# Performance work log

Hardware: AMD Instinct MI355X
Metric: run time of the kernel (lower is better)

## Reference

```python
import jax, jax.numpy as jnp
import numpy as np

WIN = 8          # current_window
PRETRAIN = 8     # pretrain_window
HEADS = 8
SHIFT = WIN // 2 # shift_size, shift_dir = [1, 1] (shift_mode=1)
L = WIN * WIN
LOG100 = float(np.log(100.0))


def _shift_mask(H, W):
    # bands (shift_dir=[1,1], no padding). Pairs from different regions get -100.
    hr = np.repeat(np.arange(3), [H - WIN, WIN - SHIFT, SHIFT])
    wr = np.repeat(np.arange(3), [W - WIN, WIN - SHIFT, SHIFT])
    region = hr[:, None] * 3 + wr[None, :]                      # [H, W]
    reg = region.reshape(H // WIN, WIN, W // WIN, WIN)
    reg = reg.transpose(0, 2, 1, 3).reshape(-1, L)              # [nw, L]
    m = np.where(reg[:, :, None] != reg[:, None, :], -100.0, 0.0)
    return jnp.asarray(m, dtype=jnp.float32)[None, :, None]     # [1, nw, 1, L, L]


def _rel_bias(cpb_w1, cpb_b1, cpb_w2):
    # Swin-v2 continuous relative position bias (log-spaced coords + MLP).
    pos = np.stack(np.meshgrid(np.arange(WIN), np.arange(WIN), indexing='ij'), -1).reshape(L, 2)
    rc = (pos[:, None, :] - pos[None, :, :]).astype(np.float32)  # [L, L, 2]
    rc = rc / (PRETRAIN - 1) * 8.0
    rc = np.sign(rc) * np.log2(np.abs(rc) + 1.0) / np.log2(8.0)
    rc = jnp.asarray(rc)
    bias = jax.nn.relu(rc @ cpb_w1 + cpb_b1) @ cpb_w2            # [L, L, heads]
    bias = 16.0 * jax.nn.sigmoid(bias)
    return bias.transpose(2, 0, 1)                               # [heads, L, L]


def _l2n(a):
    # tf.math.l2_normalize with epsilon=1.55e-5
    return a * jax.lax.rsqrt(jnp.maximum(jnp.sum(a * a, -1, keepdims=True), 1.55e-5))


def setup_inputs() -> dict:
    key = jax.random.key(0)
    ks = jax.random.split(key, 6)
    B, H, W, C = 16, 128, 128, 256
    cpb = 512
    return {
        'x': jax.random.normal(ks[0], (B, H, W, C), jnp.float32),
        'qkv_w': jax.random.normal(ks[1], (C, 3 * C), jnp.float32) * 0.02,
        'q_bias': jnp.zeros((C,), jnp.float32),
        'v_bias': jnp.zeros((C,), jnp.float32),
        'scale': jnp.full((HEADS, 1, 1), np.log(10.0), jnp.float32),
        'cpb_w1': jax.random.normal(ks[2], (2, cpb), jnp.float32) * 0.02,
        'cpb_b1': jnp.zeros((cpb,), jnp.float32),
        'cpb_w2': jax.random.normal(ks[3], (cpb, HEADS), jnp.float32) * 0.02,
        'proj_w': jax.random.normal(ks[4], (C, C), jnp.float32) * 0.02,
        'proj_b': jnp.zeros((C,), jnp.float32),
    }


def reference(x, qkv_w, q_bias, v_bias, scale, cpb_w1, cpb_b1, cpb_w2, proj_w, proj_b):
    B, H, W, C = x.shape
    units = C // HEADS
    # qkv 1x1 conv + (q, 0, v) bias
    bias = jnp.concatenate([q_bias, jnp.zeros_like(q_bias), v_bias])
    qkv = jnp.einsum('bhwc,cd->bhwd', x, qkv_w) + bias
    # cyclic shift (H, W > window so shift is applied; no padding needed)
    qkv = jnp.roll(qkv, (-SHIFT, -SHIFT), axis=(1, 2))
    # fused window partition -> [B, nw, heads, L, 3*units]
    nh, nw = H // WIN, W // WIN
    t = qkv.reshape(B, nh, WIN, nw, WIN, HEADS, 3 * units)
    t = t.transpose(0, 1, 3, 5, 2, 4, 6).reshape(B, nh * nw, HEADS, L, 3 * units)
    q, k, v = jnp.split(t, 3, axis=-1)
    # cosine attention with clamped learned logit scale
    logit_scale = jnp.exp(jnp.minimum(scale, LOG100))            # [heads, 1, 1]
    attn = jnp.einsum('bnhld,bnhmd->bnhlm', _l2n(q) * logit_scale, _l2n(k))
    attn = attn + _rel_bias(cpb_w1, cpb_b1, cpb_w2)[None, None] + _shift_mask(H, W)
    attn = jax.nn.softmax(attn, axis=-1)
    out = jnp.einsum('bnhlm,bnhmd->bnhld', attn, v)
    # reverse partition, reverse shift, output projection
    out = out.reshape(B, nh, nw, HEADS, WIN, WIN, units)
    out = out.transpose(0, 1, 4, 2, 5, 3, 6).reshape(B, H, W, C)
    out = jnp.roll(out, (SHIFT, SHIFT), axis=(1, 2))
    return jnp.einsum('bhwc,cd->bhwd', out, proj_w) + proj_b
```

## Files before the change

kernel.cpp:

```cpp
#include <hip/hip_runtime.h>

typedef __attribute__((ext_vector_type(4))) float  f32x4;
typedef __attribute__((ext_vector_type(8))) __bf16 bf16x8;
typedef __attribute__((ext_vector_type(4))) __bf16 bf16x4;

__global__ __launch_bounds__(256) void wprep_kernel(const float* __restrict__ qw,
                                                    const float* __restrict__ pw,
                                                    const float* __restrict__ qb,
                                                    const float* __restrict__ vb,
                                                    __bf16* __restrict__ W2,
                                                    __bf16* __restrict__ Wp,
                                                    float* __restrict__ bcat) {
  int i = blockIdx.x * 256 + threadIdx.x;
  if (i < 24576) {
    int h = i / 3072, rem = i - h * 3072;
    int ft = rem >> 9, rem2 = rem & 511;
    int ks = rem2 >> 6, l = rem2 & 63;
    int g = l >> 4, c = l & 15;
    int col = h * 96 + ft * 16 + c;
    bf16x8 v;
    #pragma unroll
    for (int j = 0; j < 8; ++j)
      v[j] = (__bf16)qw[(ks * 32 + g * 8 + j) * 768 + col];
    *(bf16x8*)(W2 + (size_t)i * 8) = v;
  } else if (i < 24576 + 8192) {
    int j = i - 24576;
    int wv = j >> 10, rem = j & 1023;
    int ft = rem >> 9, rem2 = rem & 511;
    int ks = rem2 >> 6, l = rem2 & 63;
    int g = l >> 4, c = l & 15;
    int col = wv * 32 + ft * 16 + c;
    bf16x8 v;
    #pragma unroll
    for (int j8 = 0; j8 < 8; ++j8)
      v[j8] = (__bf16)pw[(ks * 32 + g * 8 + j8) * 256 + col];
    *(bf16x8*)(Wp + (size_t)j * 8) = v;
  } else if (i < 24576 + 8192 + 768) {
    int cdx = i - 24576 - 8192;
    bcat[cdx] = (cdx < 256) ? qb[cdx] : ((cdx < 512) ? 0.0f : vb[cdx - 512]);
  }
}

__global__ __launch_bounds__(256) void cpb_kernel(const float* __restrict__ w1,
                                                  const float* __restrict__ b1,
                                                  const float* __restrict__ w2,
                                                  float* __restrict__ bias) {
  int pair = blockIdx.x * 256 + threadIdx.x;
  int lq = pair >> 6, mk = pair & 63;
  float d0 = (float)((lq >> 3) - (mk >> 3));
  float d1 = (float)((lq & 7) - (mk & 7));
  float v0 = d0 * (8.0f / 7.0f);
  float v1 = d1 * (8.0f / 7.0f);
  float s0 = (v0 > 0.f) ? 1.f : ((v0 < 0.f) ? -1.f : 0.f);
  float s1 = (v1 > 0.f) ? 1.f : ((v1 < 0.f) ? -1.f : 0.f);
  float r0 = s0 * log2f(fabsf(v0) + 1.0f) * (1.0f / 3.0f);
  float r1 = s1 * log2f(fabsf(v1) + 1.0f) * (1.0f / 3.0f);
  float acc[8] = {0.f, 0.f, 0.f, 0.f, 0.f, 0.f, 0.f, 0.f};
  #pragma unroll 4
  for (int j = 0; j < 512; ++j) {
    float h = fmaxf(r0 * w1[j] + r1 * w1[512 + j] + b1[j], 0.0f);
    #pragma unroll
    for (int q = 0; q < 8; ++q) acc[q] += h * w2[j * 8 + q];
  }
  #pragma unroll
  for (int q = 0; q < 8; ++q) {
    float s = 16.0f / (1.0f + __expf(-acc[q]));
    bias[(q * 64 + lq) * 64 + mk] = s;
  }
}

__device__ __forceinline__ int win_region(int tok, int wi, int wj) {
  int r = tok >> 3, cc = tok & 7;
  int rh = (wi == 15) ? ((r < 4) ? 1 : 2) : 0;
  int rw = (wj == 15) ? ((cc < 4) ? 1 : 2) : 0;
  return rh * 3 + rw;
}

__global__ __launch_bounds__(512, 2) void fused_kernel(
    const float* __restrict__ x, const __bf16* __restrict__ W2,
    const __bf16* __restrict__ Wp, const float* __restrict__ bcat,
    const float* __restrict__ scale, const float* __restrict__ cpb,
    const float* __restrict__ pb, float* __restrict__ outf)
{
  __shared__ __align__(16) __bf16 xs[64 * 256];
  __shared__ __align__(16) __bf16 vst[8][64 * 36];
  const f32x4 zz = {0.f, 0.f, 0.f, 0.f};

  int t = threadIdx.x;
  int h = t >> 6, l = t & 63, g = l >> 4, c = l & 15;
  int win = blockIdx.x, b = blockIdx.y;
  int wi = win >> 4, wj = win & 15;
  bool edge = (wi == 15) || (wj == 15);

  {
    int r = t >> 3;
    int q8 = t & 7;
    int ht = (wi * 8 + (r >> 3) + 4) & 127;
    int wt = (wj * 8 + (r & 7) + 4) & 127;
    const float* src = x + (size_t)((b * 128 + ht) * 128 + wt) * 256 + q8 * 32;
    #pragma unroll
    for (int q = 0; q < 4; ++q) {
      f32x4 a0 = *(const f32x4*)(src + q * 8);
      f32x4 a1 = *(const f32x4*)(src + q * 8 + 4);
      bf16x8 v;
      #pragma unroll
      for (int j = 0; j < 4; ++j) { v[j] = (__bf16)a0[j]; v[4 + j] = (__bf16)a1[j]; }
      int phys = (q8 * 4 + q) ^ (r & 7);
      *(bf16x8*)&xs[r * 256 + phys * 8] = v;
    }
  }
  __syncthreads();

  int toko[4];
  #pragma unroll
  for (int i = 0; i < 4; ++i) {
    int tok = 16 * i + c;
    int ht = (wi * 8 + (tok >> 3) + 4) & 127;
    int wt = (wj * 8 + (tok & 7) + 4) & 127;
    toko[i] = ((b * 128 + ht) * 128 + wt) * 256;
  }

  const __bf16* Wh = W2 + (size_t)h * 24576;
  float ls = __expf(fminf(scale[h], 4.6051701859880914f));

  bf16x8 kA[4], qB[4];
  {
    f32x4 aqk[4][4];
    #pragma unroll
    for (int ft = 0; ft < 4; ++ft)
      #pragma unroll
      for (int tt = 0; tt < 4; ++tt) aqk[ft][tt] = zz;

    #pragma unroll
    for (int ks = 0; ks < 8; ++ks) {
      bf16x8 wf[4], xf[4];
      #pragma unroll
      for (int ft = 0; ft < 4; ++ft)
        wf[ft] = *(const bf16x8*)(Wh + (size_t)((ft * 8 + ks) * 64 + l) * 8);
      #pragma unroll
      for (int tt = 0; tt < 4; ++tt) {
        int phys = (ks * 4 + g) ^ (c & 7);
        xf[tt] = *(const bf16x8*)&xs[(tt * 16 + c) * 256 + phys * 8];
      }
      #pragma unroll
      for (int ft = 0; ft < 4; ++ft)
        #pragma unroll
        for (int tt = 0; tt < 4; ++tt)
          aqk[ft][tt] = __builtin_amdgcn_mfma_f32_16x16x32_bf16(wf[ft], xf[tt], aqk[ft][tt], 0, 0, 0);
    }

    #pragma unroll
    for (int ft = 0; ft < 4; ++ft) {
      f32x4 bb = *(const f32x4*)&bcat[h * 96 + ft * 16 + 4 * g];
      #pragma unroll
      for (int tt = 0; tt < 4; ++tt) aqk[ft][tt] += bb;
    }

    #pragma unroll
    for (int tt = 0; tt < 4; ++tt) {
      float sq = 0.f, sk = 0.f;
      #pragma unroll
      for (int i = 0; i < 4; ++i) {
        sq += aqk[0][tt][i] * aqk[0][tt][i] + aqk[1][tt][i] * aqk[1][tt][i];
        sk += aqk[2][tt][i] * aqk[2][tt][i] + aqk[3][tt][i] * aqk[3][tt][i];
      }
      sq += __shfl_xor(sq, 16); sq += __shfl_xor(sq, 32);
      sk += __shfl_xor(sk, 16); sk += __shfl_xor(sk, 32);
      float rq = rsqrtf(fmaxf(sq, 1.55e-5f)) * ls;
      float rk = rsqrtf(fmaxf(sk, 1.55e-5f));
      #pragma unroll
      for (int i = 0; i < 4; ++i) {
        qB[tt][i]     = (__bf16)(aqk[0][tt][i] * rq);
        qB[tt][4 + i] = (__bf16)(aqk[1][tt][i] * rq);
        kA[tt][i]     = (__bf16)(aqk[2][tt][i] * rk);
        kA[tt][4 + i] = (__bf16)(aqk[3][tt][i] * rk);
      }
    }
  }

  {
    f32x4 av[2][4];
    #pragma unroll
    for (int ft = 0; ft < 2; ++ft)
      #pragma unroll
      for (int tt = 0; tt < 4; ++tt) av[ft][tt] = zz;

    #pragma unroll
    for (int ks = 0; ks < 8; ++ks) {
      bf16x8 wf[2], xf[4];
      #pragma unroll
      for (int ft = 0; ft < 2; ++ft)
        wf[ft] = *(const bf16x8*)(Wh + (size_t)(((4 + ft) * 8 + ks) * 64 + l) * 8);
      #pragma unroll
      for (int tt = 0; tt < 4; ++tt) {
        int phys = (ks * 4 + g) ^ (c & 7);
        xf[tt] = *(const bf16x8*)&xs[(tt * 16 + c) * 256 + phys * 8];
      }
      #pragma unroll
      for (int ft = 0; ft < 2; ++ft)
        #pragma unroll
        for (int tt = 0; tt < 4; ++tt)
          av[ft][tt] = __builtin_amdgcn_mfma_f32_16x16x32_bf16(wf[ft], xf[tt], av[ft][tt], 0, 0, 0);
    }
    __syncthreads();

    f32x4 bb4 = *(const f32x4*)&bcat[h * 96 + 64 + 4 * g];
    f32x4 bb5 = *(const f32x4*)&bcat[h * 96 + 80 + 4 * g];
    #pragma unroll
    for (int tt = 0; tt < 4; ++tt) {
      bf16x4 v0, v1;
      #pragma unroll
      for (int i = 0; i < 4; ++i) {
        v0[i] = (__bf16)(av[0][tt][i] + bb4[i]);
        v1[i] = (__bf16)(av[1][tt][i] + bb5[i]);
      }
      __bf16* vrow = &vst[h][(tt * 16 + c) * 36];
      *(bf16x4*)&vrow[4 * g]      = v0;
      *(bf16x4*)&vrow[16 + 4 * g] = v1;
    }
  }

  bf16x8 va[2][2];
  #pragma unroll
  for (int mh = 0; mh < 2; ++mh)
    #pragma unroll
    for (int kp = 0; kp < 2; ++kp)
      #pragma unroll
      for (int j = 0; j < 8; ++j)
        va[mh][kp][j] =
            vst[h][(32 * kp + 16 * (j >> 2) + 4 * g + (j & 3)) * 36 + 16 * mh + c];

  #pragma unroll
  for (int nt = 0; nt < 4; ++nt) {
    f32x4 tt4[4];
    #pragma unroll
    for (int mt = 0; mt < 4; ++mt)
      tt4[mt] = __builtin_amdgcn_mfma_f32_16x16x32_bf16(kA[mt], qB[nt], zz, 0, 0, 0);
    int q = nt * 16 + c;
    float p[16];
    #pragma unroll
    for (int mt = 0; mt < 4; ++mt) {
      f32x4 bb = *(const f32x4*)&cpb[(h * 64 + q) * 64 + mt * 16 + 4 * g];
      #pragma unroll
      for (int i = 0; i < 4; ++i) p[mt * 4 + i] = tt4[mt][i] + bb[i];
    }
    if (edge) {
      int regq = win_region(q, wi, wj);
      #pragma unroll
      for (int mt = 0; mt < 4; ++mt)
        #pragma unroll
        for (int i = 0; i < 4; ++i) {
          int k = mt * 16 + 4 * g + i;
          if (win_region(k, wi, wj) != regq) p[mt * 4 + i] -= 100.0f;
        }
    }
    float mx = -1e30f;
    #pragma unroll
    for (int j = 0; j < 16; ++j) mx = fmaxf(mx, p[j]);
    mx = fmaxf(mx, __shfl_xor(mx, 16));
    mx = fmaxf(mx, __shfl_xor(mx, 32));
    float sum = 0.f;
    #pragma unroll
    for (int j = 0; j < 16; ++j) { p[j] = __expf(p[j] - mx); sum += p[j]; }
    sum += __shfl_xor(sum, 16); sum += __shfl_xor(sum, 32);
    float rinv = 1.0f / sum;
    bf16x8 pf0, pf1;
    #pragma unroll
    for (int j = 0; j < 8; ++j) { pf0[j] = (__bf16)p[j]; pf1[j] = (__bf16)p[8 + j]; }
    #pragma unroll
    for (int mh = 0; mh < 2; ++mh) {
      f32x4 oo = __builtin_amdgcn_mfma_f32_16x16x32_bf16(va[mh][0], pf0, zz, 0, 0, 0);
      oo = __builtin_amdgcn_mfma_f32_16x16x32_bf16(va[mh][1], pf1, oo, 0, 0, 0);
      int chunk = h * 4 + 2 * mh + (g >> 1);
      int tok = nt * 16 + c;
      int phys = chunk ^ (tok & 7);
      bf16x4 ov = { (__bf16)(oo[0] * rinv), (__bf16)(oo[1] * rinv),
                    (__bf16)(oo[2] * rinv), (__bf16)(oo[3] * rinv) };
      *(bf16x4*)&xs[tok * 256 + phys * 8 + 4 * (g & 1)] = ov;
    }
  }
  __syncthreads();

  f32x4 acc2[2][4];
  #pragma unroll
  for (int ft = 0; ft < 2; ++ft)
    #pragma unroll
    for (int tt = 0; tt < 4; ++tt) acc2[ft][tt] = zz;

  const __bf16* Wph = Wp + (size_t)h * 8192;
  #pragma unroll
  for (int ks = 0; ks < 8; ++ks) {
    bf16x8 wf[2], xf[4];
    #pragma unroll
    for (int ft = 0; ft < 2; ++ft)
      wf[ft] = *(const bf16x8*)(Wph + (size_t)((ft * 8 + ks) * 64 + l) * 8);
    #pragma unroll
    for (int tt = 0; tt < 4; ++tt) {
      int phys = (ks * 4 + g) ^ (c & 7);
      xf[tt] = *(const bf16x8*)&xs[(tt * 16 + c) * 256 + phys * 8];
    }
    #pragma unroll
    for (int ft = 0; ft < 2; ++ft)
      #pragma unroll
      for (int tt = 0; tt < 4; ++tt)
        acc2[ft][tt] = __builtin_amdgcn_mfma_f32_16x16x32_bf16(wf[ft], xf[tt], acc2[ft][tt], 0, 0, 0);
  }

  #pragma unroll
  for (int ft = 0; ft < 2; ++ft) {
    f32x4 bb = *(const f32x4*)&pb[h * 32 + ft * 16 + 4 * g];
    #pragma unroll
    for (int tt = 0; tt < 4; ++tt) {
      f32x4 res = acc2[ft][tt] + bb;
      *(f32x4*)&outf[toko[tt] + h * 32 + ft * 16 + 4 * g] = res;
    }
  }
}

extern "C" void kernel_launch(void* const* d_in, const int* in_sizes, int n_in,
                              void* d_out, int out_size, void* d_ws, size_t ws_size,
                              hipStream_t stream)
{
  const float* x      = (const float*)d_in[0];
  const float* qkv_w  = (const float*)d_in[1];
  const float* q_bias = (const float*)d_in[2];
  const float* v_bias = (const float*)d_in[3];
  const float* scale  = (const float*)d_in[4];
  const float* cpb_w1 = (const float*)d_in[5];
  const float* cpb_b1 = (const float*)d_in[6];
  const float* cpb_w2 = (const float*)d_in[7];
  const float* proj_w = (const float*)d_in[8];
  const float* proj_b = (const float*)d_in[9];

  char* ws = (char*)d_ws;
  __bf16* W2   = (__bf16*)(ws);
  __bf16* Wp   = (__bf16*)(ws + 393216LL);
  float*  bcat = (float*) (ws + 524288LL);
  float*  cpb  = (float*) (ws + 527360LL);

  wprep_kernel<<<131, 256, 0, stream>>>(qkv_w, proj_w, q_bias, v_bias, W2, Wp, bcat);
  cpb_kernel<<<16, 256, 0, stream>>>(cpb_w1, cpb_b1, cpb_w2, cpb);
  fused_kernel<<<dim3(256, 16), 512, 0, stream>>>(x, W2, Wp, bcat, scale, cpb,
                                                  proj_b, (float*)d_out);
}
```

Measured before the change: 448.0 us.

## Split QK projection into per-matrix passes and merge prep kernels

The Q and K projections were computed together in one pass holding a 4x4 accumulator array. They are now done as separate two-tile passes through a shared helper, with each result normalised right away. This cuts peak accumulator register pressure under the 512-thread, 2-blocks-per-CU launch bound, at the cost of reading the x tile from shared memory again. The weight-prep and relative-position-bias kernels are also merged into a single launch to save one kernel launch.

```diff
diff --git a/kernel.cpp b/kernel.cpp
--- a/kernel.cpp
+++ b/kernel.cpp
@@ -4,68 +4,66 @@
 typedef __attribute__((ext_vector_type(8))) __bf16 bf16x8;
 typedef __attribute__((ext_vector_type(4))) __bf16 bf16x4;
 
-__global__ __launch_bounds__(256) void wprep_kernel(const float* __restrict__ qw,
-                                                    const float* __restrict__ pw,
-                                                    const float* __restrict__ qb,
-                                                    const float* __restrict__ vb,
-                                                    __bf16* __restrict__ W2,
-                                                    __bf16* __restrict__ Wp,
-                                                    float* __restrict__ bcat) {
-  int i = blockIdx.x * 256 + threadIdx.x;
-  if (i < 24576) {
-    int h = i / 3072, rem = i - h * 3072;
-    int ft = rem >> 9, rem2 = rem & 511;
-    int ks = rem2 >> 6, l = rem2 & 63;
-    int g = l >> 4, c = l & 15;
-    int col = h * 96 + ft * 16 + c;
-    bf16x8 v;
-    #pragma unroll
-    for (int j = 0; j < 8; ++j)
-      v[j] = (__bf16)qw[(ks * 32 + g * 8 + j) * 768 + col];
-    *(bf16x8*)(W2 + (size_t)i * 8) = v;
-  } else if (i < 24576 + 8192) {
-    int j = i - 24576;
-    int wv = j >> 10, rem = j & 1023;
-    int ft = rem >> 9, rem2 = rem & 511;
-    int ks = rem2 >> 6, l = rem2 & 63;
-    int g = l >> 4, c = l & 15;
-    int col = wv * 32 + ft * 16 + c;
-    bf16x8 v;
-    #pragma unroll
-    for (int j8 = 0; j8 < 8; ++j8)
-      v[j8] = (__bf16)pw[(ks * 32 + g * 8 + j8) * 256 + col];
-    *(bf16x8*)(Wp + (size_t)j * 8) = v;
-  } else if (i < 24576 + 8192 + 768) {
-    int cdx = i - 24576 - 8192;
-    bcat[cdx] = (cdx < 256) ? qb[cdx] : ((cdx < 512) ? 0.0f : vb[cdx - 512]);
-  }
-}
-
-__global__ __launch_bounds__(256) void cpb_kernel(const float* __restrict__ w1,
-                                                  const float* __restrict__ b1,
-                                                  const float* __restrict__ w2,
-                                                  float* __restrict__ bias) {
-  int pair = blockIdx.x * 256 + threadIdx.x;
-  int lq = pair >> 6, mk = pair & 63;
-  float d0 = (float)((lq >> 3) - (mk >> 3));
-  float d1 = (float)((lq & 7) - (mk & 7));
-  float v0 = d0 * (8.0f / 7.0f);
-  float v1 = d1 * (8.0f / 7.0f);
-  float s0 = (v0 > 0.f) ? 1.f : ((v0 < 0.f) ? -1.f : 0.f);
-  float s1 = (v1 > 0.f) ? 1.f : ((v1 < 0.f) ? -1.f : 0.f);
-  float r0 = s0 * log2f(fabsf(v0) + 1.0f) * (1.0f / 3.0f);
-  float r1 = s1 * log2f(fabsf(v1) + 1.0f) * (1.0f / 3.0f);
-  float acc[8] = {0.f, 0.f, 0.f, 0.f, 0.f, 0.f, 0.f, 0.f};
-  #pragma unroll 4
-  for (int j = 0; j < 512; ++j) {
-    float h = fmaxf(r0 * w1[j] + r1 * w1[512 + j] + b1[j], 0.0f);
-    #pragma unroll
-    for (int q = 0; q < 8; ++q) acc[q] += h * w2[j * 8 + q];
-  }
-  #pragma unroll
-  for (int q = 0; q < 8; ++q) {
-    float s = 16.0f / (1.0f + __expf(-acc[q]));
-    bias[(q * 64 + lq) * 64 + mk] = s;
+__global__ __launch_bounds__(256) void prep_kernel(
+    const float* __restrict__ qw, const float* __restrict__ pw,
+    const float* __restrict__ qb, const float* __restrict__ vb,
+    const float* __restrict__ w1, const float* __restrict__ b1,
+    const float* __restrict__ w2,
+    __bf16* __restrict__ W2, __bf16* __restrict__ Wp,
+    float* __restrict__ bcat, float* __restrict__ cpbias)
+{
+  if (blockIdx.x < 131) {
+    int i = blockIdx.x * 256 + threadIdx.x;
+    if (i < 24576) {
+      int h = i / 3072, rem = i - h * 3072;
+      int ft = rem >> 9, rem2 = rem & 511;
+      int ks = rem2 >> 6, l = rem2 & 63;
+      int g = l >> 4, c = l & 15;
+      int col = h * 96 + ft * 16 + c;
+      bf16x8 v;
+      #pragma unroll
+      for (int j = 0; j < 8; ++j)
+        v[j] = (__bf16)qw[(ks * 32 + g * 8 + j) * 768 + col];
+      *(bf16x8*)(W2 + (size_t)i * 8) = v;
+    } else if (i < 24576 + 8192) {
+      int j = i - 24576;
+      int wv = j >> 10, rem = j & 1023;
+      int ft = rem >> 9, rem2 = rem & 511;
+      int ks = rem2 >> 6, l = rem2 & 63;
+      int g = l >> 4, c = l & 15;
+      int col = wv * 32 + ft * 16 + c;
+      bf16x8 v;
+      #pragma unroll
+      for (int j8 = 0; j8 < 8; ++j8)
+        v[j8] = (__bf16)pw[(ks * 32 + g * 8 + j8) * 256 + col];
+      *(bf16x8*)(Wp + (size_t)j * 8) = v;
+    } else if (i < 24576 + 8192 + 768) {
+      int cdx = i - 24576 - 8192;
+      bcat[cdx] = (cdx < 256) ? qb[cdx] : ((cdx < 512) ? 0.0f : vb[cdx - 512]);
+    }
+  } else {
+    int pair = (blockIdx.x - 131) * 256 + threadIdx.x;
+    int lq = pair >> 6, mk = pair & 63;
+    float d0 = (float)((lq >> 3) - (mk >> 3));
+    float d1 = (float)((lq & 7) - (mk & 7));
+    float v0 = d0 * (8.0f / 7.0f);
+    float v1 = d1 * (8.0f / 7.0f);
+    float s0 = (v0 > 0.f) ? 1.f : ((v0 < 0.f) ? -1.f : 0.f);
+    float s1 = (v1 > 0.f) ? 1.f : ((v1 < 0.f) ? -1.f : 0.f);
+    float r0 = s0 * log2f(fabsf(v0) + 1.0f) * (1.0f / 3.0f);
+    float r1 = s1 * log2f(fabsf(v1) + 1.0f) * (1.0f / 3.0f);
+    float acc[8] = {0.f, 0.f, 0.f, 0.f, 0.f, 0.f, 0.f, 0.f};
+    #pragma unroll 4
+    for (int j = 0; j < 512; ++j) {
+      float h = fmaxf(r0 * w1[j] + r1 * w1[512 + j] + b1[j], 0.0f);
+      #pragma unroll
+      for (int q = 0; q < 8; ++q) acc[q] += h * w2[j * 8 + q];
+    }
+    #pragma unroll
+    for (int q = 0; q < 8; ++q) {
+      float s = 16.0f / (1.0f + __expf(-acc[q]));
+      cpbias[(q * 64 + lq) * 64 + mk] = s;
+    }
   }
 }
 
@@ -74,6 +72,30 @@
   int rh = (wi == 15) ? ((r < 4) ? 1 : 2) : 0;
   int rw = (wj == 15) ? ((cc < 4) ? 1 : 2) : 0;
   return rh * 3 + rw;
+}
+
+template <int FT>
+__device__ __forceinline__ void qkv2(const __bf16* __restrict__ Wh,
+                                     const __bf16* xs, int l, int g, int c,
+                                     f32x4 (&a)[2][4])
+{
+  const f32x4 zz = {0.f, 0.f, 0.f, 0.f};
+  #pragma unroll
+  for (int ft = 0; ft < 2; ++ft)
+    #pragma unroll
+    for (int tt = 0; tt < 4; ++tt) a[ft][tt] = zz;
+  #pragma unroll
+  for (int ks = 0; ks < 8; ++ks) {
+    bf16x8 w0 = *(const bf16x8*)(Wh + (size_t)(((FT + 0) * 8 + ks) * 64 + l) * 8);
+    bf16x8 w1 = *(const bf16x8*)(Wh + (size_t)(((FT + 1) * 8 + ks) * 64 + l) * 8);
+    #pragma unroll
+    for (int tt = 0; tt < 4; ++tt) {
+      int phys = (ks * 4 + g) ^ (c & 7);
+      bf16x8 xf = *(const bf16x8*)&xs[(tt * 16 + c) * 256 + phys * 8];
+      a[0][tt] = __builtin_amdgcn_mfma_f32_16x16x32_bf16(w0, xf, a[0][tt], 0, 0, 0);
+      a[1][tt] = __builtin_amdgcn_mfma_f32_16x16x32_bf16(w1, xf, a[1][tt], 0, 0, 0);
+    }
+  }
 }
 
 __global__ __launch_bounds__(512, 2) void fused_kernel(
@@ -123,96 +145,64 @@
   const __bf16* Wh = W2 + (size_t)h * 24576;
   float ls = __expf(fminf(scale[h], 4.6051701859880914f));
 
-  bf16x8 kA[4], qB[4];
+  bf16x8 qB[4], kA[4];
   {
-    f32x4 aqk[4][4];
-    #pragma unroll
-    for (int ft = 0; ft < 4; ++ft)
-      #pragma unroll
-      for (int tt = 0; tt < 4; ++tt) aqk[ft][tt] = zz;
-
-    #pragma unroll
-    for (int ks = 0; ks < 8; ++ks) {
-      bf16x8 wf[4], xf[4];
-      #pragma unroll
-      for (int ft = 0; ft < 4; ++ft)
-        wf[ft] = *(const bf16x8*)(Wh + (size_t)((ft * 8 + ks) * 64 + l) * 8);
-      #pragma unroll
-      for (int tt = 0; tt < 4; ++tt) {
-        int phys = (ks * 4 + g) ^ (c & 7);
-        xf[tt] = *(const bf16x8*)&xs[(tt * 16 + c) * 256 + phys * 8];
+    f32x4 a[2][4];
+    qkv2<0>(Wh, xs, l, g, c, a);
+    f32x4 b0 = *(const f32x4*)&bcat[h * 96 + 0  + 4 * g];
+    f32x4 b1 = *(const f32x4*)&bcat[h * 96 + 16 + 4 * g];
+    #pragma unroll
+    for (int tt = 0; tt < 4; ++tt) {
+      a[0][tt] += b0; a[1][tt] += b1;
+      float s = 0.f;
+      #pragma unroll
+      for (int i = 0; i < 4; ++i)
+        s += a[0][tt][i] * a[0][tt][i] + a[1][tt][i] * a[1][tt][i];
+      s += __shfl_xor(s, 16); s += __shfl_xor(s, 32);
+      float r = rsqrtf(fmaxf(s, 1.55e-5f)) * ls;
+      #pragma unroll
+      for (int i = 0; i < 4; ++i) {
+        qB[tt][i]     = (__bf16)(a[0][tt][i] * r);
+        qB[tt][4 + i] = (__bf16)(a[1][tt][i] * r);
       }
-      #pragma unroll
-      for (int ft = 0; ft < 4; ++ft)
-        #pragma unroll
-        for (int tt = 0; tt < 4; ++tt)
-          aqk[ft][tt] = __builtin_amdgcn_mfma_f32_16x16x32_bf16(wf[ft], xf[tt], aqk[ft][tt], 0, 0, 0);
-    }
-
-    #pragma unroll
-    for (int ft = 0; ft < 4; ++ft) {
-      f32x4 bb = *(const f32x4*)&bcat[h * 96 + ft * 16 + 4 * g];
-      #pragma unroll
-      for (int tt = 0; tt < 4; ++tt) aqk[ft][tt] += bb;
-    }
-
-    #pragma unroll
-    for (int tt = 0; tt < 4; ++tt) {
-      float sq = 0.f, sk = 0.f;
+    }
+  }
+
+  {
+    f32x4 a[2][4];
+    qkv2<2>(Wh, xs, l, g, c, a);
+    f32x4 b0 = *(const f32x4*)&bcat[h * 96 + 32 + 4 * g];
+    f32x4 b1 = *(const f32x4*)&bcat[h * 96 + 48 + 4 * g];
+    #pragma unroll
+    for (int tt = 0; tt < 4; ++tt) {
+      a[0][tt] += b0; a[1][tt] += b1;
+      float s = 0.f;
+      #pragma unroll
+      for (int i = 0; i < 4; ++i)
+        s += a[0][tt][i] * a[0][tt][i] + a[1][tt][i] * a[1][tt][i];
+      s += __shfl_xor(s, 16); s += __shfl_xor(s, 32);
+      float r = rsqrtf(fmaxf(s, 1.55e-5f));
       #pragma unroll
       for (int i = 0; i < 4; ++i) {
-        sq += aqk[0][tt][i] * aqk[0][tt][i] + aqk[1][tt][i] * aqk[1][tt][i];
-        sk += aqk[2][tt][i] * aqk[2][tt][i] + aqk[3][tt][i] * aqk[3][tt][i];
+        kA[tt][i]     = (__bf16)(a[0][tt][i] * r);
+        kA[tt][4 + i] = (__bf16)(a[1][tt][i] * r);
       }
-      sq += __shfl_xor(sq, 16); sq += __shfl_xor(sq, 32);
-      sk += __shfl_xor(sk, 16); sk += __shfl_xor(sk, 32);
-      float rq = rsqrtf(fmaxf(sq, 1.55e-5f)) * ls;
-      float rk = rsqrtf(fmaxf(sk, 1.55e-5f));
+    }
+  }
+
+  {
+    f32x4 a[2][4];
+    qkv2<4>(Wh, xs, l, g, c, a);
+    __syncthreads();
+    f32x4 b0 = *(const f32x4*)&bcat[h * 96 + 64 + 4 * g];
+    f32x4 b1 = *(const f32x4*)&bcat[h * 96 + 80 + 4 * g];
+    #pragma unroll
+    for (int tt = 0; tt < 4; ++tt) {
+      bf16x4 v0, v1;
       #pragma unroll
       for (int i = 0; i < 4; ++i) {
-        qB[tt][i]     = (__bf16)(aqk[0][tt][i] * rq);
-        qB[tt][4 + i] = (__bf16)(aqk[1][tt][i] * rq);
-        kA[tt][i]     = (__bf16)(aqk[2][tt][i] * rk);
-        kA[tt][4 + i] = (__bf16)(aqk[3][tt][i] * rk);
-      }
-    }
-  }
-
-  {
-    f32x4 av[2][4];
-    #pragma unroll
-    for (int ft = 0; ft < 2; ++ft)
-      #pragma unroll
-      for (int tt = 0; tt < 4; ++tt) av[ft][tt] = zz;
-
-    #pragma unroll
-    for (int ks = 0; ks < 8; ++ks) {
-      bf16x8 wf[2], xf[4];
-      #pragma unroll
-      for (int ft = 0; ft < 2; ++ft)
-        wf[ft] = *(const bf16x8*)(Wh + (size_t)(((4 + ft) * 8 + ks) * 64 + l) * 8);
-      #pragma unroll
-      for (int tt = 0; tt < 4; ++tt) {
-        int phys = (ks * 4 + g) ^ (c & 7);
-        xf[tt] = *(const bf16x8*)&xs[(tt * 16 + c) * 256 + phys * 8];
-      }
-      #pragma unroll
-      for (int ft = 0; ft < 2; ++ft)
-        #pragma unroll
-        for (int tt = 0; tt < 4; ++tt)
-          av[ft][tt] = __builtin_amdgcn_mfma_f32_16x16x32_bf16(wf[ft], xf[tt], av[ft][tt], 0, 0, 0);
-    }
-    __syncthreads();
-
-    f32x4 bb4 = *(const f32x4*)&bcat[h * 96 + 64 + 4 * g];
-    f32x4 bb5 = *(const f32x4*)&bcat[h * 96 + 80 + 4 * g];
-    #pragma unroll
-    for (int tt = 0; tt < 4; ++tt) {
-      bf16x4 v0, v1;
-      #pragma unroll
-      for (int i = 0; i < 4; ++i) {
-        v0[i] = (__bf16)(av[0][tt][i] + bb4[i]);
-        v1[i] = (__bf16)(av[1][tt][i] + bb5[i]);
+        v0[i] = (__bf16)(a[0][tt][i] + b0[i]);
+        v1[i] = (__bf16)(a[1][tt][i] + b1[i]);
       }
       __bf16* vrow = &vst[h][(tt * 16 + c) * 36];
       *(bf16x4*)&vrow[4 * g]      = v0;
@@ -290,20 +280,15 @@
   const __bf16* Wph = Wp + (size_t)h * 8192;
   #pragma unroll
   for (int ks = 0; ks < 8; ++ks) {
-    bf16x8 wf[2], xf[4];
-    #pragma unroll
-    for (int ft = 0; ft < 2; ++ft)
-      wf[ft] = *(const bf16x8*)(Wph + (size_t)((ft * 8 + ks) * 64 + l) * 8);
+    bf16x8 w0 = *(const bf16x8*)(Wph + (size_t)((0 * 8 + ks) * 64 + l) * 8);
+    bf16x8 w1 = *(const bf16x8*)(Wph + (size_t)((1 * 8 + ks) * 64 + l) * 8);
     #pragma unroll
     for (int tt = 0; tt < 4; ++tt) {
       int phys = (ks * 4 + g) ^ (c & 7);
-      xf[tt] = *(const bf16x8*)&xs[(tt * 16 + c) * 256 + phys * 8];
-    }
-    #pragma unroll
-    for (int ft = 0; ft < 2; ++ft)
-      #pragma unroll
-      for (int tt = 0; tt < 4; ++tt)
-        acc2[ft][tt] = __builtin_amdgcn_mfma_f32_16x16x32_bf16(wf[ft], xf[tt], acc2[ft][tt], 0, 0, 0);
+      bf16x8 xf = *(const bf16x8*)&xs[(tt * 16 + c) * 256 + phys * 8];
+      acc2[0][tt] = __builtin_amdgcn_mfma_f32_16x16x32_bf16(w0, xf, acc2[0][tt], 0, 0, 0);
+      acc2[1][tt] = __builtin_amdgcn_mfma_f32_16x16x32_bf16(w1, xf, acc2[1][tt], 0, 0, 0);
+    }
   }
 
   #pragma unroll
@@ -338,8 +323,8 @@
   float*  bcat = (float*) (ws + 524288LL);
   float*  cpb  = (float*) (ws + 527360LL);
 
-  wprep_kernel<<<131, 256, 0, stream>>>(qkv_w, proj_w, q_bias, v_bias, W2, Wp, bcat);
-  cpb_kernel<<<16, 256, 0, stream>>>(cpb_w1, cpb_b1, cpb_w2, cpb);
+  prep_kernel<<<147, 256, 0, stream>>>(qkv_w, proj_w, q_bias, v_bias,
+                                       cpb_w1, cpb_b1, cpb_w2, W2, Wp, bcat, cpb);
   fused_kernel<<<dim3(256, 16), 512, 0, stream>>>(x, W2, Wp, bcat, scale, cpb,
                                                   proj_b, (float*)d_out);
 }
```

Result: no change. 444.8 us (-0.7%).
